# Kernel optimization log

Measured on AMD Instinct MI355X. Metric: run time of the kernel, lower is better.

Reference implementation:

```python
import jax, jax.numpy as jnp
import numpy as np

B, D, H, E, K = 8192, 1024, 4096, 8, 2
LOSS_COEF = 0.01
EPS_COMBINE = float(np.finfo(np.float64).eps)  # np.finfo(float).eps used in combine


def setup_inputs() -> dict:
    key = jax.random.key(0)
    ks = jax.random.split(key, 6)
    s_in = 1.0 / np.sqrt(D)
    s_hid = 1.0 / np.sqrt(H)
    return {
        "x": jax.random.normal(ks[0], (B, D), jnp.float32),
        "w_gate": jax.random.uniform(ks[1], (E, D), jnp.float32, -s_in, s_in),
        "fc1_w": jax.random.uniform(ks[2], (E, H, D), jnp.float32, -s_in, s_in),
        "fc1_b": jax.random.uniform(ks[3], (E, H), jnp.float32, -s_in, s_in),
        "fc2_w": jax.random.uniform(ks[4], (E, D, H), jnp.float32, -s_hid, s_hid),
        "fc2_b": jax.random.uniform(ks[5], (E, D), jnp.float32, -s_hid, s_hid),
    }


def _cv_squared(v):
    # torch .var() uses ddof=1
    return jnp.var(v, ddof=1) / (jnp.mean(v) ** 2 + 1e-10)


def _top_k_gating(x, w_gate):
    # clean logits (noisy_gating=False): [B, E]
    logits = x @ w_gate.T
    top_vals, top_idx = jax.lax.top_k(logits, K + 1)  # min(k+1, E)
    topk_vals = top_vals[:, :K]
    topk_idx = top_idx[:, :K]
    topk_gates = jax.nn.softmax(topk_vals, axis=1)
    gates = jnp.zeros((x.shape[0], E), x.dtype)
    gates = gates.at[jnp.arange(x.shape[0])[:, None], topk_idx].set(topk_gates)
    return gates


def _forward(x, w_gate, fc1_w, fc1_b, fc2_w, fc2_b):
    gates = _top_k_gating(x, w_gate)            # [B, E], sparse (k nonzeros/row)
    importance = gates.sum(axis=0)              # [E]
    load = (gates > 0).sum(axis=0).astype(jnp.float32)
    loss = (_cv_squared(importance) + _cv_squared(load)) * LOSS_COEF

    # Dense-equivalent expert compute: tokens with gate==0 contribute 0 to the
    # combine, identical math to SparseDispatcher's gather/scatter.
    h = jnp.einsum('bd,ehd->beh', x, fc1_w) + fc1_b            # [B, E, H]
    h = jax.nn.gelu(h, approximate=False)                      # torch exact gelu
    o = jnp.einsum('beh,edh->bed', h, fc2_w) + fc2_b           # [B, E, D]
    log_p = jax.nn.log_softmax(o, axis=-1)                     # LogSoftmax(dim=1)

    # combine: exp, weight by gates, scatter-add, eps-fill, log
    combined = jnp.einsum('be,bed->bd', gates, jnp.exp(log_p)) # [B, D]
    combined = jnp.where(combined == 0, EPS_COMBINE, combined)
    y = jnp.log(combined)
    return y, loss


def reference(x, w_gate, fc1_w, fc1_b, fc2_w, fc2_b):
    return _forward(x, w_gate, fc1_w, fc1_b, fc2_w, fc2_b)
```

## Files before the change

kernel.cpp:

```cpp
#include <hip/hip_runtime.h>
#include <cstdint>
#include <cmath>

#define BT 8192
#define DD 1024
#define HH 4096
#define EE 8
#define MTMAX 136

typedef __attribute__((ext_vector_type(8))) short short8;
typedef __attribute__((ext_vector_type(4))) float f32x4;
typedef unsigned short u16;
typedef unsigned int u32;

__device__ __forceinline__ u16 f2bf(float f) {
    u32 u = __float_as_uint(f);
    u += 0x7FFFu + ((u >> 16) & 1u);
    return (u16)(u >> 16);
}

__device__ __forceinline__ void gld_lds16(const void* g, void* l) {
    __builtin_amdgcn_global_load_lds((__attribute__((address_space(1))) void*)g,
                                     (__attribute__((address_space(3))) void*)l,
                                     16, 0, 0);
}

__global__ void cvt_kernel(const float* __restrict__ src, u16* __restrict__ dst, int n8) {
    int i = blockIdx.x * blockDim.x + threadIdx.x;
    if (i >= n8) return;
    size_t base = (size_t)i * 8;
    float4 a = *(const float4*)(src + base);
    float4 b = *(const float4*)(src + base + 4);
    uint4 o;
    o.x = (u32)f2bf(a.x) | ((u32)f2bf(a.y) << 16);
    o.y = (u32)f2bf(a.z) | ((u32)f2bf(a.w) << 16);
    o.z = (u32)f2bf(b.x) | ((u32)f2bf(b.y) << 16);
    o.w = (u32)f2bf(b.z) | ((u32)f2bf(b.w) << 16);
    *(uint4*)(dst + base) = o;
}

__global__ void gating_kernel(const float* __restrict__ x, const float* __restrict__ wg,
                              float* __restrict__ gate_arr, int* __restrict__ list,
                              int* __restrict__ info,
                              int* __restrict__ counts, float* __restrict__ importance) {
    int wave = (blockIdx.x * blockDim.x + threadIdx.x) >> 6;
    int lane = threadIdx.x & 63;
    if (wave >= BT) return;
    const float* xr = x + (size_t)wave * DD;
    double acc[EE];
#pragma unroll
    for (int e = 0; e < EE; ++e) acc[e] = 0.0;
    for (int i = lane; i < DD; i += 64) {
        double xv = (double)xr[i];
#pragma unroll
        for (int e = 0; e < EE; ++e)
            acc[e] += xv * (double)wg[e * DD + i];
    }
#pragma unroll
    for (int e = 0; e < EE; ++e) {
        double v = acc[e];
        for (int off = 32; off; off >>= 1) v += __shfl_down(v, off, 64);
        acc[e] = v;
    }
    if (lane == 0) {
        int i0 = 0; double v0 = acc[0];
        for (int e = 1; e < EE; ++e) if (acc[e] > v0) { v0 = acc[e]; i0 = e; }
        int i1 = -1; double v1 = -1e300;
        for (int e = 0; e < EE; ++e) { if (e == i0) continue; if (acc[e] > v1) { v1 = acc[e]; i1 = e; } }
        double e1 = exp(v1 - v0);
        double s = 1.0 + e1;
        float g0 = (float)(1.0 / s);
        float g1 = (float)(e1 / s);
        gate_arr[2 * wave]     = g0;
        gate_arr[2 * wave + 1] = g1;
        atomicAdd(&importance[i0], g0);
        atomicAdd(&importance[i1], g1);
        int p0 = atomicAdd(&counts[i0], 1);
        list[i0 * BT + p0] = wave;
        int p1 = atomicAdd(&counts[i1], 1);
        list[i1 * BT + p1] = wave;
        info[2 * wave]     = (i0 << 16) | p0;
        info[2 * wave + 1] = (i1 << 16) | p1;
    }
}

__global__ void loss_kernel(const int* __restrict__ counts, const float* __restrict__ importance,
                            int* __restrict__ offs, float* __restrict__ out_loss,
                            int* __restrict__ tmap, int* __restrict__ ntiles) {
    if (threadIdx.x == 0 && blockIdx.x == 0) {
        double mi = 0, ml = 0;
        int off = 0;
        for (int e = 0; e < EE; e++) {
            offs[e] = off; off += counts[e];
            mi += (double)importance[e]; ml += (double)counts[e];
        }
        mi /= EE; ml /= EE;
        double vi = 0, vl = 0;
        for (int e = 0; e < EE; e++) {
            double di = (double)importance[e] - mi; vi += di * di;
            double dl = (double)counts[e] - ml;     vl += dl * dl;
        }
        vi /= (EE - 1); vl /= (EE - 1);
        double cv_i = vi / (mi * mi + 1e-10);
        double cv_l = vl / (ml * ml + 1e-10);
        *out_loss = (float)((cv_i + cv_l) * 0.01);
        int ntl = 0;
        for (int e = 0; e < EE; e++)
            for (int t = 0; t < counts[e]; t += 128)
                tmap[ntl++] = (e << 20) | t;
        *ntiles = ntl;
    }
}

__global__ void gather_x_kernel(const float* __restrict__ x, const int* __restrict__ list,
                                const int* __restrict__ counts, const int* __restrict__ offs,
                                u16* __restrict__ xg) {
    int r = blockIdx.x;
    int e = 0;
#pragma unroll
    for (int i = 1; i < EE; ++i) if (r >= offs[i]) e = i;
    int m = r - offs[e];
    if (m >= counts[e]) return;
    int token = list[e * BT + m];
    const float* src = x + (size_t)token * DD;
    u16* dst = xg + (size_t)r * DD;
    int i = threadIdx.x * 4;
    float4 a = *(const float4*)(src + i);
    uint2 o;
    o.x = (u32)f2bf(a.x) | ((u32)f2bf(a.y) << 16);
    o.y = (u32)f2bf(a.z) | ((u32)f2bf(a.w) << 16);
    *(uint2*)(dst + i) = o;
}

template <int K, int NT, bool GELU, bool GATHER>
__global__ __launch_bounds__(256) void moe_gemm(const u16* __restrict__ Asrc,
                                                const u16* __restrict__ Bsrc,
                                                const float* __restrict__ bias,
                                                const int* __restrict__ list,
                                                const int* __restrict__ counts,
                                                const int* __restrict__ offs,
                                                const int* __restrict__ tmap,
                                                const int* __restrict__ ntiles,
                                                u16* __restrict__ outB,
                                                float* __restrict__ outF) {
    constexpr int NXT = NT / 128;
    constexpr int nwg = NXT * MTMAX;
    constexpr int q = nwg / 8;
    const int bid = blockIdx.x;
    const int wg = (bid & 7) * q + (bid >> 3);
    const int nt = wg / MTMAX;
    const int mt = wg - nt * MTMAX;
    if (mt >= *ntiles) return;
    const int ent = tmap[mt];
    const int e = ent >> 20;
    const int mbase = ent & 0xFFFFF;
    const int cnt = counts[e];
    const int mmax = cnt - mbase;
    const int rowbase = offs[e] + mbase;
    const int nbase = nt * 128;
    const int tid = threadIdx.x;
    const int lane = tid & 63;
    const int wv = tid >> 6;

    __shared__ u16 As0[128 * 32], As1[128 * 32];
    __shared__ u16 Bs0[128 * 32], Bs1[128 * 32];
    __shared__ int rows_lds[128];

    if constexpr (GATHER) {
        if (tid < 128) {
            int m = min(tid, mmax - 1);
            rows_lds[tid] = list[e * BT + mbase + m];
        }
        __syncthreads();
    }

    const int myrow = tid & 127;
    const int kch = tid >> 7;
    size_t arow;
    if constexpr (GATHER) arow = (size_t)rows_lds[myrow];
    else                  arow = (size_t)(rowbase + min(myrow, mmax - 1));
    const u16* aptr = Asrc + arow * (size_t)K + kch * 8;
    const u16* bptr = Bsrc + ((size_t)e * NT + nbase + myrow) * (size_t)K + kch * 8;

    f32x4 acc[4][4] = {};
    const int moff = (wv >> 1) * 64;
    const int noff = (wv & 1) * 64;
    const int kq = lane >> 4;
    const int rsub = lane & 15;

#define STAGE(Ad, Bd, k0)                                        \
    do {                                                         \
        gld_lds16(aptr + (k0),      &(Ad)[tid * 8]);             \
        gld_lds16(aptr + (k0) + 16, &(Ad)[(tid + 256) * 8]);     \
        gld_lds16(bptr + (k0),      &(Bd)[tid * 8]);             \
        gld_lds16(bptr + (k0) + 16, &(Bd)[(tid + 256) * 8]);     \
    } while (0)

#define COMPUTE(Ad, Bd)                                                              \
    do {                                                                             \
        short8 af[4], bfr[4];                                                        \
        _Pragma("unroll")                                                            \
        for (int mi = 0; mi < 4; mi++)                                               \
            af[mi] = *(const short8*)&(Ad)[(kq * 128 + moff + mi * 16 + rsub) * 8];  \
        _Pragma("unroll")                                                            \
        for (int ni = 0; ni < 4; ni++)                                               \
            bfr[ni] = *(const short8*)&(Bd)[(kq * 128 + noff + ni * 16 + rsub) * 8]; \
        _Pragma("unroll")                                                            \
        for (int mi = 0; mi < 4; mi++)                                               \
            _Pragma("unroll")                                                        \
            for (int ni = 0; ni < 4; ni++)                                           \
                acc[mi][ni] = __builtin_amdgcn_mfma_f32_16x16x32_bf16(                \
                    af[mi], bfr[ni], acc[mi][ni], 0, 0, 0);                          \
    } while (0)

    STAGE(As0, Bs0, 0);
    __syncthreads();
    for (int k0 = 0; k0 < K; k0 += 64) {
        STAGE(As1, Bs1, k0 + 32);
        COMPUTE(As0, Bs0);
        __syncthreads();
        if (k0 + 64 < K) STAGE(As0, Bs0, k0 + 64);
        COMPUTE(As1, Bs1);
        __syncthreads();
    }
#undef STAGE
#undef COMPUTE

    const int rq = (lane >> 4) * 4;
    float bvals[4];
#pragma unroll
    for (int ni = 0; ni < 4; ni++)
        bvals[ni] = bias[(size_t)e * NT + nbase + noff + ni * 16 + rsub];
#pragma unroll
    for (int mi = 0; mi < 4; mi++) {
#pragma unroll
        for (int r = 0; r < 4; r++) {
            int m = moff + mi * 16 + rq + r;
            if (m < mmax) {
                size_t ro = (size_t)(rowbase + m);
#pragma unroll
                for (int ni = 0; ni < 4; ni++) {
                    int n = nbase + noff + ni * 16 + rsub;
                    float v = acc[mi][ni][r] + bvals[ni];
                    if constexpr (GELU) {
                        v = 0.5f * v * (1.0f + erff(v * 0.7071067811865476f));
                        outB[ro * NT + n] = f2bf(v);
                    } else {
                        outF[ro * NT + n] = v;
                    }
                }
            }
        }
    }
}

__global__ void combine_kernel(const float* __restrict__ o, const float* __restrict__ gates,
                               const int* __restrict__ info, const int* __restrict__ offs,
                               float* __restrict__ y) {
    const int b = blockIdx.x;
    const int tid = threadIdx.x;
    const int lane = tid & 63, wv = tid >> 6;
    const int inf0 = info[2 * b], inf1 = info[2 * b + 1];
    const int r0i = offs[inf0 >> 16] + (inf0 & 0xffff);
    const int r1i = offs[inf1 >> 16] + (inf1 & 0xffff);
    const float* r0 = o + (size_t)r0i * DD;
    const float* r1 = o + (size_t)r1i * DD;
    float v0[4], v1[4];
#pragma unroll
    for (int j = 0; j < 4; j++) { v0[j] = r0[tid + 256 * j]; v1[j] = r1[tid + 256 * j]; }
    float m0 = fmaxf(fmaxf(v0[0], v0[1]), fmaxf(v0[2], v0[3]));
    float m1 = fmaxf(fmaxf(v1[0], v1[1]), fmaxf(v1[2], v1[3]));
#pragma unroll
    for (int off = 32; off; off >>= 1) {
        m0 = fmaxf(m0, __shfl_xor(m0, off, 64));
        m1 = fmaxf(m1, __shfl_xor(m1, off, 64));
    }
    __shared__ float sred[2][4];
    if (lane == 0) { sred[0][wv] = m0; sred[1][wv] = m1; }
    __syncthreads();
    m0 = fmaxf(fmaxf(sred[0][0], sred[0][1]), fmaxf(sred[0][2], sred[0][3]));
    m1 = fmaxf(fmaxf(sred[1][0], sred[1][1]), fmaxf(sred[1][2], sred[1][3]));
    float p0[4], p1[4], s0 = 0.f, s1 = 0.f;
#pragma unroll
    for (int j = 0; j < 4; j++) {
        p0[j] = expf(v0[j] - m0); s0 += p0[j];
        p1[j] = expf(v1[j] - m1); s1 += p1[j];
    }
#pragma unroll
    for (int off = 32; off; off >>= 1) {
        s0 += __shfl_xor(s0, off, 64);
        s1 += __shfl_xor(s1, off, 64);
    }
    __shared__ float sred2[2][4];
    if (lane == 0) { sred2[0][wv] = s0; sred2[1][wv] = s1; }
    __syncthreads();
    s0 = sred2[0][0] + sred2[0][1] + sred2[0][2] + sred2[0][3];
    s1 = sred2[1][0] + sred2[1][1] + sred2[1][2] + sred2[1][3];
    const float c0 = gates[2 * b] / s0;
    const float c1 = gates[2 * b + 1] / s1;
#pragma unroll
    for (int j = 0; j < 4; j++) {
        float c = p0[j] * c0 + p1[j] * c1;
        if (c == 0.f) c = 2.2204460492503131e-16f;
        y[(size_t)b * DD + tid + 256 * j] = logf(c);
    }
}

extern "C" void kernel_launch(void* const* d_in, const int* in_sizes, int n_in,
                              void* d_out, int out_size, void* d_ws, size_t ws_size,
                              hipStream_t stream) {
    const float* x     = (const float*)d_in[0];
    const float* wgate = (const float*)d_in[1];
    const float* fc1w  = (const float*)d_in[2];
    const float* fc1b  = (const float*)d_in[3];
    const float* fc2w  = (const float*)d_in[4];
    const float* fc2b  = (const float*)d_in[5];
    float* out = (float*)d_out;

    char* ws = (char*)d_ws;
    const size_t MB = 1024 * 1024;
    const bool big = ws_size >= 289 * MB;
    u16* w1b = (u16*)(ws);
    float* o = (float*)(ws);
    u16* w2b = (u16*)(ws + 64 * MB);
    u16* xb  = (u16*)(ws + 128 * MB);
    u16* h   = (u16*)(ws + (big ? 128 : 144) * MB);
    u16* xg  = (u16*)(ws + 256 * MB);
    char* meta = ws + (big ? 288 : 272) * MB;
    int* counts       = (int*)meta;
    int* offs         = (int*)(meta + 32);
    float* importance = (float*)(meta + 64);
    int* ntiles       = (int*)(meta + 96);
    float* gate_arr   = (float*)(meta + 128);
    int* info         = (int*)(meta + 128 + 65536);
    int* list         = (int*)(meta + 128 + 131072);
    int* tmap         = (int*)(meta + 512 * 1024);

    hipMemsetAsync(meta, 0, 96, stream);
    cvt_kernel<<<(EE * HH * DD / 8 + 255) / 256, 256, 0, stream>>>(fc1w, w1b, EE * HH * DD / 8);
    cvt_kernel<<<(EE * DD * HH / 8 + 255) / 256, 256, 0, stream>>>(fc2w, w2b, EE * DD * HH / 8);
    gating_kernel<<<BT / 4, 256, 0, stream>>>(x, wgate, gate_arr, list, info, counts, importance);
    loss_kernel<<<1, 64, 0, stream>>>(counts, importance, offs, out + (size_t)BT * DD, tmap, ntiles);

    if (big) {
        gather_x_kernel<<<2 * BT, 256, 0, stream>>>(x, list, counts, offs, xg);
        moe_gemm<DD, HH, true, false><<<(HH / 128) * MTMAX, 256, 0, stream>>>(
            xg, w1b, fc1b, nullptr, counts, offs, tmap, ntiles, h, nullptr);
    } else {
        cvt_kernel<<<(BT * DD / 8 + 255) / 256, 256, 0, stream>>>(x, xb, BT * DD / 8);
        moe_gemm<DD, HH, true, true><<<(HH / 128) * MTMAX, 256, 0, stream>>>(
            xb, w1b, fc1b, list, counts, offs, tmap, ntiles, h, nullptr);
    }
    moe_gemm<HH, DD, false, false><<<(DD / 128) * MTMAX, 256, 0, stream>>>(
        h, w2b, fc2b, nullptr, counts, offs, tmap, ntiles, nullptr, o);
    combine_kernel<<<BT, 256, 0, stream>>>(o, gate_arr, info, offs, out);
}
```

Measured before the change: 1.320 ms.

## Deepen MoE GEMM LDS pipeline to four stages and remap XCD tile schedule

The GEMM's main loop moves from double-buffered LDS staging with full __syncthreads to a four-buffer ring: three k-steps are in flight, and explicit vmcnt waits plus s_barrier replace the syncs. The aim is to hide global-load latency better and cut barrier stalls. The workgroup-to-tile mapping now gives each XCD a contiguous range of N tiles, interleaved in groups of eight M tiles, to improve L2 reuse of weights. The gating kernel switches to float4 vectorized loads. LDS use doubles, which may lower occupancy.

```diff
diff --git a/kernel.cpp b/kernel.cpp
--- a/kernel.cpp
+++ b/kernel.cpp
@@ -50,11 +50,17 @@
     double acc[EE];
 #pragma unroll
     for (int e = 0; e < EE; ++e) acc[e] = 0.0;
-    for (int i = lane; i < DD; i += 64) {
-        double xv = (double)xr[i];
-#pragma unroll
-        for (int e = 0; e < EE; ++e)
-            acc[e] += xv * (double)wg[e * DD + i];
+#pragma unroll
+    for (int c = 0; c < DD / 256; ++c) {
+        const int i = c * 256 + lane * 4;
+        float4 xv = *(const float4*)(xr + i);
+        double x0 = xv.x, x1 = xv.y, x2 = xv.z, x3 = xv.w;
+#pragma unroll
+        for (int e = 0; e < EE; ++e) {
+            float4 wv = *(const float4*)(wg + e * DD + i);
+            acc[e] += x0 * (double)wv.x + x1 * (double)wv.y
+                    + x2 * (double)wv.z + x3 * (double)wv.w;
+        }
     }
 #pragma unroll
     for (int e = 0; e < EE; ++e) {
@@ -144,12 +150,15 @@
                                                 u16* __restrict__ outB,
                                                 float* __restrict__ outF) {
     constexpr int NXT = NT / 128;
-    constexpr int nwg = NXT * MTMAX;
-    constexpr int q = nwg / 8;
+    constexpr int C = NXT / 8;
+    constexpr int q = C * MTMAX;
     const int bid = blockIdx.x;
-    const int wg = (bid & 7) * q + (bid >> 3);
-    const int nt = wg / MTMAX;
-    const int mt = wg - nt * MTMAX;
+    const int xcd = bid & 7;
+    const int j = bid >> 3;
+    const int st = j / (8 * C);
+    const int w = j - st * 8 * C;
+    const int nt = xcd * C + (w >> 3);
+    const int mt = st * 8 + (w & 7);
     if (mt >= *ntiles) return;
     const int ent = tmap[mt];
     const int e = ent >> 20;
@@ -162,8 +171,8 @@
     const int lane = tid & 63;
     const int wv = tid >> 6;
 
-    __shared__ u16 As0[128 * 32], As1[128 * 32];
-    __shared__ u16 Bs0[128 * 32], Bs1[128 * 32];
+    __shared__ u16 As[4][128 * 32];
+    __shared__ u16 Bs[4][128 * 32];
     __shared__ int rows_lds[128];
 
     if constexpr (GATHER) {
@@ -188,41 +197,61 @@
     const int kq = lane >> 4;
     const int rsub = lane & 15;
 
-#define STAGE(Ad, Bd, k0)                                        \
+#define STAGE(bi, k0)                                            \
     do {                                                         \
-        gld_lds16(aptr + (k0),      &(Ad)[tid * 8]);             \
-        gld_lds16(aptr + (k0) + 16, &(Ad)[(tid + 256) * 8]);     \
-        gld_lds16(bptr + (k0),      &(Bd)[tid * 8]);             \
-        gld_lds16(bptr + (k0) + 16, &(Bd)[(tid + 256) * 8]);     \
+        gld_lds16(aptr + (k0),      &As[bi][tid * 8]);           \
+        gld_lds16(aptr + (k0) + 16, &As[bi][(tid + 256) * 8]);   \
+        gld_lds16(bptr + (k0),      &Bs[bi][tid * 8]);           \
+        gld_lds16(bptr + (k0) + 16, &Bs[bi][(tid + 256) * 8]);   \
     } while (0)
 
-#define COMPUTE(Ad, Bd)                                                              \
-    do {                                                                             \
-        short8 af[4], bfr[4];                                                        \
-        _Pragma("unroll")                                                            \
-        for (int mi = 0; mi < 4; mi++)                                               \
-            af[mi] = *(const short8*)&(Ad)[(kq * 128 + moff + mi * 16 + rsub) * 8];  \
-        _Pragma("unroll")                                                            \
-        for (int ni = 0; ni < 4; ni++)                                               \
-            bfr[ni] = *(const short8*)&(Bd)[(kq * 128 + noff + ni * 16 + rsub) * 8]; \
-        _Pragma("unroll")                                                            \
-        for (int mi = 0; mi < 4; mi++)                                               \
-            _Pragma("unroll")                                                        \
-            for (int ni = 0; ni < 4; ni++)                                           \
-                acc[mi][ni] = __builtin_amdgcn_mfma_f32_16x16x32_bf16(                \
-                    af[mi], bfr[ni], acc[mi][ni], 0, 0, 0);                          \
+#define COMPUTE(bi)                                                                   \
+    do {                                                                              \
+        short8 af[4], bfr[4];                                                         \
+        _Pragma("unroll")                                                             \
+        for (int mi = 0; mi < 4; mi++)                                                \
+            af[mi] = *(const short8*)&As[bi][(kq * 128 + moff + mi * 16 + rsub) * 8]; \
+        _Pragma("unroll")                                                             \
+        for (int ni = 0; ni < 4; ni++)                                                \
+            bfr[ni] = *(const short8*)&Bs[bi][(kq * 128 + noff + ni * 16 + rsub) * 8];\
+        _Pragma("unroll")                                                             \
+        for (int mi = 0; mi < 4; mi++)                                                \
+            _Pragma("unroll")                                                         \
+            for (int ni = 0; ni < 4; ni++)                                            \
+                acc[mi][ni] = __builtin_amdgcn_mfma_f32_16x16x32_bf16(                 \
+                    af[mi], bfr[ni], acc[mi][ni], 0, 0, 0);                           \
     } while (0)
 
-    STAGE(As0, Bs0, 0);
-    __syncthreads();
-    for (int k0 = 0; k0 < K; k0 += 64) {
-        STAGE(As1, Bs1, k0 + 32);
-        COMPUTE(As0, Bs0);
-        __syncthreads();
-        if (k0 + 64 < K) STAGE(As0, Bs0, k0 + 64);
-        COMPUTE(As1, Bs1);
-        __syncthreads();
-    }
+#define PHASE(cb, sb, tt)                                            \
+    do {                                                             \
+        if ((tt) + 3 < NSTEPS) {                                     \
+            asm volatile("s_waitcnt vmcnt(8)" ::: "memory");         \
+            __builtin_amdgcn_s_barrier();                            \
+            STAGE(sb, ((tt) + 3) * 32);                              \
+        } else if ((tt) + 2 < NSTEPS) {                              \
+            asm volatile("s_waitcnt vmcnt(8)" ::: "memory");         \
+            __builtin_amdgcn_s_barrier();                            \
+        } else if ((tt) + 1 < NSTEPS) {                              \
+            asm volatile("s_waitcnt vmcnt(4)" ::: "memory");         \
+            __builtin_amdgcn_s_barrier();                            \
+        } else {                                                     \
+            asm volatile("s_waitcnt vmcnt(0)" ::: "memory");         \
+            __builtin_amdgcn_s_barrier();                            \
+        }                                                            \
+        COMPUTE(cb);                                                 \
+    } while (0)
+
+    constexpr int NSTEPS = K / 32;
+    STAGE(0, 0);
+    STAGE(1, 32);
+    STAGE(2, 64);
+    for (int t = 0; t < NSTEPS; t += 4) {
+        PHASE(0, 3, t);
+        PHASE(1, 0, t + 1);
+        PHASE(2, 1, t + 2);
+        PHASE(3, 2, t + 3);
+    }
+#undef PHASE
 #undef STAGE
 #undef COMPUTE
 
```

Result: slower. 1.428 ms (+8.2%).

## Enlarge MoE GEMM tiles to 256x256 with 512 threads; vectorize gating loads

Applied to the files above, without the earlier changes.

The grouped expert GEMMs move from 128x128 tiles with 256 threads to 256x256 tiles with 512 threads. Each wave now computes a 128x64 sub-tile with 8x4 MFMA accumulators, the LDS staging layout is reindexed, and the tile map steps by 256 rows. This raises arithmetic intensity per byte loaded from global memory and LDS. In exchange it costs more registers and LDS per block, gives fewer blocks, and wastes more work on padded partial tiles per expert. The gating dot product also switches to float4 loads.

```diff
diff --git a/kernel.cpp b/kernel.cpp
--- a/kernel.cpp
+++ b/kernel.cpp
@@ -6,7 +6,7 @@
 #define DD 1024
 #define HH 4096
 #define EE 8
-#define MTMAX 136
+#define MT2 72
 
 typedef __attribute__((ext_vector_type(8))) short short8;
 typedef __attribute__((ext_vector_type(4))) float f32x4;
@@ -50,11 +50,17 @@
     double acc[EE];
 #pragma unroll
     for (int e = 0; e < EE; ++e) acc[e] = 0.0;
-    for (int i = lane; i < DD; i += 64) {
-        double xv = (double)xr[i];
-#pragma unroll
-        for (int e = 0; e < EE; ++e)
-            acc[e] += xv * (double)wg[e * DD + i];
+#pragma unroll
+    for (int c = 0; c < DD / 256; ++c) {
+        const int i = c * 256 + lane * 4;
+        float4 xv = *(const float4*)(xr + i);
+        double x0 = xv.x, x1 = xv.y, x2 = xv.z, x3 = xv.w;
+#pragma unroll
+        for (int e = 0; e < EE; ++e) {
+            float4 wv = *(const float4*)(wg + e * DD + i);
+            acc[e] += x0 * (double)wv.x + x1 * (double)wv.y
+                    + x2 * (double)wv.z + x3 * (double)wv.w;
+        }
     }
 #pragma unroll
     for (int e = 0; e < EE; ++e) {
@@ -106,7 +112,7 @@
         *out_loss = (float)((cv_i + cv_l) * 0.01);
         int ntl = 0;
         for (int e = 0; e < EE; e++)
-            for (int t = 0; t < counts[e]; t += 128)
+            for (int t = 0; t < counts[e]; t += 256)
                 tmap[ntl++] = (e << 20) | t;
         *ntiles = ntl;
     }
@@ -133,7 +139,7 @@
 }
 
 template <int K, int NT, bool GELU, bool GATHER>
-__global__ __launch_bounds__(256) void moe_gemm(const u16* __restrict__ Asrc,
+__global__ __launch_bounds__(512) void moe_gemm(const u16* __restrict__ Asrc,
                                                 const u16* __restrict__ Bsrc,
                                                 const float* __restrict__ bias,
                                                 const int* __restrict__ list,
@@ -143,13 +149,13 @@
                                                 const int* __restrict__ ntiles,
                                                 u16* __restrict__ outB,
                                                 float* __restrict__ outF) {
-    constexpr int NXT = NT / 128;
-    constexpr int nwg = NXT * MTMAX;
+    constexpr int NXT = NT / 256;
+    constexpr int nwg = NXT * MT2;
     constexpr int q = nwg / 8;
     const int bid = blockIdx.x;
     const int wg = (bid & 7) * q + (bid >> 3);
-    const int nt = wg / MTMAX;
-    const int mt = wg - nt * MTMAX;
+    const int nt = wg / MT2;
+    const int mt = wg - nt * MT2;
     if (mt >= *ntiles) return;
     const int ent = tmap[mt];
     const int e = ent >> 20;
@@ -157,56 +163,56 @@
     const int cnt = counts[e];
     const int mmax = cnt - mbase;
     const int rowbase = offs[e] + mbase;
-    const int nbase = nt * 128;
+    const int nbase = nt * 256;
     const int tid = threadIdx.x;
     const int lane = tid & 63;
     const int wv = tid >> 6;
 
-    __shared__ u16 As0[128 * 32], As1[128 * 32];
-    __shared__ u16 Bs0[128 * 32], Bs1[128 * 32];
-    __shared__ int rows_lds[128];
+    __shared__ u16 As0[256 * 32], As1[256 * 32];
+    __shared__ u16 Bs0[256 * 32], Bs1[256 * 32];
+    __shared__ int rows_lds[256];
 
     if constexpr (GATHER) {
-        if (tid < 128) {
+        if (tid < 256) {
             int m = min(tid, mmax - 1);
             rows_lds[tid] = list[e * BT + mbase + m];
         }
         __syncthreads();
     }
 
-    const int myrow = tid & 127;
-    const int kch = tid >> 7;
+    const int myrow = tid & 255;
+    const int kch = tid >> 8;
     size_t arow;
     if constexpr (GATHER) arow = (size_t)rows_lds[myrow];
     else                  arow = (size_t)(rowbase + min(myrow, mmax - 1));
     const u16* aptr = Asrc + arow * (size_t)K + kch * 8;
     const u16* bptr = Bsrc + ((size_t)e * NT + nbase + myrow) * (size_t)K + kch * 8;
 
-    f32x4 acc[4][4] = {};
-    const int moff = (wv >> 1) * 64;
-    const int noff = (wv & 1) * 64;
+    f32x4 acc[8][4] = {};
+    const int moff = (wv >> 2) * 128;
+    const int noff = (wv & 3) * 64;
     const int kq = lane >> 4;
     const int rsub = lane & 15;
 
-#define STAGE(Ad, Bd, k0)                                        \
-    do {                                                         \
-        gld_lds16(aptr + (k0),      &(Ad)[tid * 8]);             \
-        gld_lds16(aptr + (k0) + 16, &(Ad)[(tid + 256) * 8]);     \
-        gld_lds16(bptr + (k0),      &(Bd)[tid * 8]);             \
-        gld_lds16(bptr + (k0) + 16, &(Bd)[(tid + 256) * 8]);     \
+#define STAGE(Ad, Bd, k0)                                              \
+    do {                                                               \
+        gld_lds16(aptr + (k0),      &(Ad)[(kch * 256 + myrow) * 8]);   \
+        gld_lds16(aptr + (k0) + 16, &(Ad)[((kch + 2) * 256 + myrow) * 8]); \
+        gld_lds16(bptr + (k0),      &(Bd)[(kch * 256 + myrow) * 8]);   \
+        gld_lds16(bptr + (k0) + 16, &(Bd)[((kch + 2) * 256 + myrow) * 8]); \
     } while (0)
 
 #define COMPUTE(Ad, Bd)                                                              \
     do {                                                                             \
-        short8 af[4], bfr[4];                                                        \
+        short8 af[8], bfr[4];                                                        \
         _Pragma("unroll")                                                            \
-        for (int mi = 0; mi < 4; mi++)                                               \
-            af[mi] = *(const short8*)&(Ad)[(kq * 128 + moff + mi * 16 + rsub) * 8];  \
+        for (int mi = 0; mi < 8; mi++)                                               \
+            af[mi] = *(const short8*)&(Ad)[(kq * 256 + moff + mi * 16 + rsub) * 8];  \
         _Pragma("unroll")                                                            \
         for (int ni = 0; ni < 4; ni++)                                               \
-            bfr[ni] = *(const short8*)&(Bd)[(kq * 128 + noff + ni * 16 + rsub) * 8]; \
+            bfr[ni] = *(const short8*)&(Bd)[(kq * 256 + noff + ni * 16 + rsub) * 8]; \
         _Pragma("unroll")                                                            \
-        for (int mi = 0; mi < 4; mi++)                                               \
+        for (int mi = 0; mi < 8; mi++)                                               \
             _Pragma("unroll")                                                        \
             for (int ni = 0; ni < 4; ni++)                                           \
                 acc[mi][ni] = __builtin_amdgcn_mfma_f32_16x16x32_bf16(                \
@@ -232,7 +238,7 @@
     for (int ni = 0; ni < 4; ni++)
         bvals[ni] = bias[(size_t)e * NT + nbase + noff + ni * 16 + rsub];
 #pragma unroll
-    for (int mi = 0; mi < 4; mi++) {
+    for (int mi = 0; mi < 8; mi++) {
 #pragma unroll
         for (int r = 0; r < 4; r++) {
             int m = moff + mi * 16 + rq + r;
@@ -344,14 +350,14 @@
 
     if (big) {
         gather_x_kernel<<<2 * BT, 256, 0, stream>>>(x, list, counts, offs, xg);
-        moe_gemm<DD, HH, true, false><<<(HH / 128) * MTMAX, 256, 0, stream>>>(
+        moe_gemm<DD, HH, true, false><<<(HH / 256) * MT2, 512, 0, stream>>>(
             xg, w1b, fc1b, nullptr, counts, offs, tmap, ntiles, h, nullptr);
     } else {
         cvt_kernel<<<(BT * DD / 8 + 255) / 256, 256, 0, stream>>>(x, xb, BT * DD / 8);
-        moe_gemm<DD, HH, true, true><<<(HH / 128) * MTMAX, 256, 0, stream>>>(
+        moe_gemm<DD, HH, true, true><<<(HH / 256) * MT2, 512, 0, stream>>>(
             xb, w1b, fc1b, list, counts, offs, tmap, ntiles, h, nullptr);
     }
-    moe_gemm<HH, DD, false, false><<<(DD / 128) * MTMAX, 256, 0, stream>>>(
+    moe_gemm<HH, DD, false, false><<<(DD / 256) * MT2, 512, 0, stream>>>(
         h, w2b, fc2b, nullptr, counts, offs, tmap, ntiles, nullptr, o);
     combine_kernel<<<BT, 256, 0, stream>>>(o, gate_arr, info, offs, out);
 }
```

New measurement: 1.308 ms. No clear change (-0.9%).
